# Performance work log

Measured on AMD Instinct MI355X. Metric: run time of the kernel, lower is better.

The kernel has to match this reference:

```python
import jax, jax.numpy as jnp
import numpy as np

N_NODES = 50000
N_EDGES = 800000
IN_DIM = 128
HID = 64
HEADS = 4
NEG_SLOPE = 0.2  # PyG GATConv default
EPS = 1e-16


def _glorot(key, shape):
    fan_in, fan_out = shape[0], shape[-1]
    lim = jnp.sqrt(6.0 / (fan_in + fan_out))
    return jax.random.uniform(key, shape, jnp.float32, -lim, lim)


def setup_inputs() -> dict:
    key = jax.random.key(0)
    ks = jax.random.split(key, 10)
    x = jax.random.normal(ks[0], (N_NODES, IN_DIM), jnp.float32)
    edge_index = jax.random.randint(ks[1], (2, N_EDGES), 0, N_NODES, jnp.int64)
    # Layer 1: in=128 -> 64 per head, 4 heads (concat -> 256)
    W1 = _glorot(ks[2], (IN_DIM, HEADS * HID))
    a_src1 = _glorot(ks[3], (HEADS, HID))
    a_dst1 = _glorot(ks[4], (HEADS, HID))
    b1 = jnp.zeros((HEADS * HID,), jnp.float32)
    # Layer 2: in=256 -> 1, 1 head
    W2 = _glorot(ks[5], (HEADS * HID, 1))
    a_src2 = _glorot(ks[6], (1, 1))
    a_dst2 = _glorot(ks[7], (1, 1))
    b2 = jnp.zeros((1,), jnp.float32)
    return {"x": x, "edge_index": edge_index, "W1": W1, "a_src1": a_src1,
            "a_dst1": a_dst1, "b1": b1, "W2": W2, "a_src2": a_src2,
            "a_dst2": a_dst2, "b2": b2}


def gat_conv(x, src, dst, W, a_src, a_dst, bias, heads, out_dim, num_nodes, concat):
    # Linear projection per head: [N, heads, out_dim]
    h = (x @ W).reshape(num_nodes, heads, out_dim)
    # Node-level attention logits: [N, heads]
    alpha_s = jnp.einsum('nhd,hd->nh', h, a_src)
    alpha_d = jnp.einsum('nhd,hd->nh', h, a_dst)
    # Per-edge score with LeakyReLU
    e = jax.nn.leaky_relu(alpha_s[src] + alpha_d[dst], NEG_SLOPE)  # [E, heads]
    # Segment softmax over incoming edges of each destination node
    e_max = jax.lax.stop_gradient(jax.ops.segment_max(e, dst, num_segments=num_nodes))
    e_exp = jnp.exp(e - e_max[dst])
    denom = jax.ops.segment_sum(e_exp, dst, num_segments=num_nodes)
    alpha = e_exp / (denom[dst] + EPS)  # [E, heads]
    # Weighted scatter-aggregate of source features
    msg = h[src] * alpha[:, :, None]  # [E, heads, out_dim]
    out = jax.ops.segment_sum(msg, dst, num_segments=num_nodes)
    if concat:
        out = out.reshape(num_nodes, heads * out_dim)
    else:
        out = out.mean(axis=1)
    return out + bias


def reference(x, edge_index, W1, a_src1, a_dst1, b1, W2, a_src2, a_dst2, b2):
    n = x.shape[0]
    loops = jnp.arange(n, dtype=edge_index.dtype)
    src = jnp.concatenate([edge_index[0], loops])  # PyG add_self_loops=True
    dst = jnp.concatenate([edge_index[1], loops])
    h = gat_conv(x, src, dst, W1, a_src1, a_dst1, b1, HEADS, HID, n, concat=True)
    h = jax.nn.relu(h)
    out = gat_conv(h, src, dst, W2, a_src2, a_dst2, b2, 1, 1, n, concat=True)
    return jax.nn.sigmoid(out)
```

## Files before the change

### kernel.cpp

```cpp
#include <hip/hip_runtime.h>
#include <hip/hip_bf16.h>

#define N_NODES 50000
#define N_EDGES 800000
#define ET      (N_EDGES + N_NODES)
#define IN_DIM  128
#define HID     64
#define HEADS   4
#define C1      (HEADS * HID)
#define NEG_SLOPE 0.2f

#define NBH     256
#define NBUCKET 196
#define SCAN_N  (NBUCKET * NBH)

typedef unsigned short ushort_t;
typedef __attribute__((ext_vector_type(8))) short bf16x8;
typedef __attribute__((ext_vector_type(4))) float f32x4;

__device__ __forceinline__ float asf(unsigned int u) {
    union { unsigned int i; float f; } c; c.i = u; return c.f;
}
__device__ __forceinline__ float bf2f(ushort_t u) {
    return asf(((unsigned int)u) << 16);
}
__device__ __forceinline__ ushort_t f2bf(float f) {
    union { float f; unsigned int i; } c; c.f = f;
    unsigned int r = c.i + 0x7fffu + ((c.i >> 16) & 1u);
    return (ushort_t)(r >> 16);
}
__device__ __forceinline__ float lrelu(float x) { return x > 0.f ? x : NEG_SLOPE * x; }

__device__ __forceinline__ float wave_sum(float v) {
    #pragma unroll
    for (int off = 32; off > 0; off >>= 1) v += __shfl_xor(v, off, 64);
    return v;
}
__device__ __forceinline__ int wave_sum_i(int v) {
    #pragma unroll
    for (int off = 32; off > 0; off >>= 1) v += __shfl_xor(v, off, 64);
    return v;
}

__device__ __forceinline__ int load_idx(const int* ei, int elem, int is64) {
    return is64 ? ei[2 * elem] : ei[elem];
}

__device__ __forceinline__ int detect64(const int* __restrict__ ei) {
    int lane = threadIdx.x & 63;
    unsigned long long nz = __ballot(lane < 32 && ei[2 * lane + 1] != 0);
    return nz == 0ull;
}

__global__ __launch_bounds__(256) void k_hist(const int* __restrict__ ei,
                                              int* __restrict__ HT,
                                              const float* __restrict__ W1,
                                              ushort_t* __restrict__ w1s) {
    __shared__ int lcnt[NBUCKET];
    int f = detect64(ei);
    if (threadIdx.x < NBUCKET) lcnt[threadIdx.x] = 0;
    if (threadIdx.x < 128) {
        int o = blockIdx.x * 128 + threadIdx.x;
        int j = o & 7, l = (o >> 3) & 63, c = (o >> 9) & 3, t = o >> 11;
        int k = c * 32 + ((l >> 4) << 3) + j;
        int n = (t << 4) + (l & 15);
        w1s[o] = f2bf(W1[k * C1 + n]);
    }
    __syncthreads();
    for (int e = blockIdx.x * 256 + threadIdx.x; e < ET; e += NBH * 256) {
        int d = (e < N_EDGES) ? load_idx(ei, N_EDGES + e, f) : e - N_EDGES;
        atomicAdd(&lcnt[d >> 8], 1);
    }
    __syncthreads();
    if (threadIdx.x < NBUCKET)
        HT[threadIdx.x * NBH + blockIdx.x] = lcnt[threadIdx.x];
}

__global__ __launch_bounds__(256) void k_blksum(const int* __restrict__ v,
                                                int* __restrict__ bsum) {
    int i = blockIdx.x * 256 + threadIdx.x;
    int s = wave_sum_i(v[i]);
    __shared__ int ws[4];
    int lane = threadIdx.x & 63, wid = threadIdx.x >> 6;
    if (lane == 0) ws[wid] = s;
    __syncthreads();
    if (threadIdx.x == 0) bsum[blockIdx.x] = ws[0] + ws[1] + ws[2] + ws[3];
}

__global__ __launch_bounds__(256) void k_bscan(const int* __restrict__ bsum,
                                               int* __restrict__ boff) {
    int tid = threadIdx.x, lane = tid & 63, wid = tid >> 6;
    int v = (tid < NBUCKET) ? bsum[tid] : 0;
    int x = v;
    #pragma unroll
    for (int off = 1; off < 64; off <<= 1) {
        int t = __shfl_up(x, off, 64);
        if (lane >= off) x += t;
    }
    __shared__ int ws[4];
    if (lane == 63) ws[wid] = x;
    __syncthreads();
    int add = 0;
    for (int w = 0; w < 4; ++w) if (w < wid) add += ws[w];
    x += add;
    if (tid < NBUCKET) boff[tid] = x - v;
}

__global__ __launch_bounds__(256) void k_apply(const int* __restrict__ v,
                                               const int* __restrict__ boff,
                                               int* __restrict__ out) {
    int i = blockIdx.x * 256 + threadIdx.x;
    int lane = threadIdx.x & 63, wid = threadIdx.x >> 6;
    int val = v[i];
    int x = val;
    #pragma unroll
    for (int off = 1; off < 64; off <<= 1) {
        int t = __shfl_up(x, off, 64);
        if (lane >= off) x += t;
    }
    __shared__ int ws[4];
    if (lane == 63) ws[wid] = x;
    __syncthreads();
    int add = boff[blockIdx.x];
    for (int w = 0; w < 4; ++w) if (w < wid) add += ws[w];
    out[i] = add + x - val;
}

__global__ __launch_bounds__(256) void k_bucket_scatter(const int* __restrict__ ei,
                                                        const int* __restrict__ HToff,
                                                        uint2* __restrict__ bucketed) {
    __shared__ int lbase[NBUCKET];
    int f = detect64(ei);
    if (threadIdx.x < NBUCKET)
        lbase[threadIdx.x] = HToff[threadIdx.x * NBH + blockIdx.x];
    __syncthreads();
    for (int e = blockIdx.x * 256 + threadIdx.x; e < ET; e += NBH * 256) {
        int s, d;
        if (e < N_EDGES) { s = load_idx(ei, e, f); d = load_idx(ei, N_EDGES + e, f); }
        else             { s = d = e - N_EDGES; }
        int pos = atomicAdd(&lbase[d >> 8], 1);
        bucketed[pos] = make_uint2((unsigned)s, (unsigned)d);
    }
}

__global__ __launch_bounds__(256) void k_fine(const uint2* __restrict__ bucketed,
                                              const int* __restrict__ HToff,
                                              int* __restrict__ row_start,
                                              int* __restrict__ edge_src) {
    __shared__ int fcnt[256];
    __shared__ int fcur[256];
    __shared__ int ws[4];
    int b = blockIdx.x, tid = threadIdx.x;
    int lane = tid & 63, wid = tid >> 6;
    int estart = HToff[b * NBH];
    int eend   = (b + 1 < NBUCKET) ? HToff[(b + 1) * NBH] : ET;
    fcnt[tid] = 0;
    __syncthreads();
    for (int i = estart + tid; i < eend; i += 256)
        atomicAdd(&fcnt[bucketed[i].y & 255], 1);
    __syncthreads();
    int v = fcnt[tid];
    int x = v;
    #pragma unroll
    for (int off = 1; off < 64; off <<= 1) {
        int t = __shfl_up(x, off, 64);
        if (lane >= off) x += t;
    }
    if (lane == 63) ws[wid] = x;
    __syncthreads();
    int add = 0;
    for (int w = 0; w < 4; ++w) if (w < wid) add += ws[w];
    int excl = add + x - v;
    int node = b * 256 + tid;
    if (node <= N_NODES) row_start[node] = estart + excl;
    fcur[tid] = estart + excl;
    __syncthreads();
    for (int i = estart + tid; i < eend; i += 256) {
        uint2 u = bucketed[i];
        int pos = atomicAdd(&fcur[u.y & 255], 1);
        edge_src[pos] = (int)u.x;
    }
}

__global__ __launch_bounds__(256) void k_gemm1(const float* __restrict__ x,
                                               const ushort_t* __restrict__ w1s,
                                               const float* __restrict__ a_src1,
                                               const float* __restrict__ a_dst1,
                                               ushort_t* __restrict__ h1,
                                               float* __restrict__ as1,
                                               float* __restrict__ ad1) {
    int lane = threadIdx.x & 63;
    int wave = (blockIdx.x * 256 + threadIdx.x) >> 6;
    int row0 = wave * 16;
    if (row0 >= N_NODES) return;
    int quad = lane >> 4, mrow = lane & 15;

    f32x4 acc[16];
    #pragma unroll
    for (int t = 0; t < 16; ++t) acc[t] = (f32x4){0.f, 0.f, 0.f, 0.f};

    const float* xrow = x + (size_t)(row0 + mrow) * IN_DIM + quad * 8;
    #pragma unroll
    for (int c = 0; c < 4; ++c) {
        float4 xa = *(const float4*)(xrow + c * 32);
        float4 xb = *(const float4*)(xrow + c * 32 + 4);
        bf16x8 a;
        a[0] = (short)f2bf(xa.x); a[1] = (short)f2bf(xa.y);
        a[2] = (short)f2bf(xa.z); a[3] = (short)f2bf(xa.w);
        a[4] = (short)f2bf(xb.x); a[5] = (short)f2bf(xb.y);
        a[6] = (short)f2bf(xb.z); a[7] = (short)f2bf(xb.w);
        #pragma unroll
        for (int t = 0; t < 16; ++t) {
            bf16x8 b = *(const bf16x8*)(w1s + (((t * 4 + c) * 64 + lane) << 3));
            acc[t] = __builtin_amdgcn_mfma_f32_16x16x32_bf16(a, b, acc[t], 0, 0, 0);
        }
    }

    #pragma unroll
    for (int t = 0; t < 16; ++t) {
        int col = t * 16 + mrow;
        #pragma unroll
        for (int r = 0; r < 4; ++r) {
            h1[(size_t)(row0 + quad * 4 + r) * C1 + col] = f2bf(acc[t][r]);
        }
    }

    float asv[16], adv[16];
    #pragma unroll
    for (int t = 0; t < 16; ++t) {
        asv[t] = a_src1[t * 16 + mrow];
        adv[t] = a_dst1[t * 16 + mrow];
    }
    #pragma unroll
    for (int r = 0; r < 4; ++r) {
        float ps[4] = {0.f, 0.f, 0.f, 0.f};
        float pd[4] = {0.f, 0.f, 0.f, 0.f};
        #pragma unroll
        for (int t = 0; t < 16; ++t) {
            ps[t >> 2] += acc[t][r] * asv[t];
            pd[t >> 2] += acc[t][r] * adv[t];
        }
        #pragma unroll
        for (int h = 0; h < 4; ++h) {
            #pragma unroll
            for (int off = 1; off < 16; off <<= 1) {
                ps[h] += __shfl_xor(ps[h], off, 64);
                pd[h] += __shfl_xor(pd[h], off, 64);
            }
        }
        if (mrow == 0) {
            int rr = row0 + quad * 4 + r;
            #pragma unroll
            for (int h = 0; h < 4; ++h) {
                as1[rr * 4 + h] = ps[h];
                ad1[rr * 4 + h] = pd[h];
            }
        }
    }
}

__global__ __launch_bounds__(256) void k_agg1(const ushort_t* __restrict__ h1,
                                              const float* __restrict__ as1,
                                              const float* __restrict__ ad1,
                                              const int* __restrict__ row_start,
                                              const int* __restrict__ edge_src,
                                              const float* __restrict__ b1,
                                              const float* __restrict__ W2,
                                              const float* __restrict__ a_src2,
                                              const float* __restrict__ a_dst2,
                                              float2* __restrict__ pk,
                                              float* __restrict__ ad2) {
    __shared__ float wbuf[4][64][4];
    int lane = threadIdx.x & 63;
    int wid  = threadIdx.x >> 6;
    int node = blockIdx.x * 4 + wid;
    int rs = row_start[node], re = row_start[node + 1];
    float4 ad = *(const float4*)&ad1[node * 4];
    const int lane32 = lane & 31;
    const int half   = lane >> 5;
    const int head8  = lane32 >> 3;

    float acc[8] = {0.f, 0.f, 0.f, 0.f, 0.f, 0.f, 0.f, 0.f};
    float4 den = make_float4(0.f, 0.f, 0.f, 0.f);

    for (int base = rs; base < re; base += 64) {
        int i = base + lane;
        int s_l = 0;
        float4 w = make_float4(0.f, 0.f, 0.f, 0.f);
        if (i < re) {
            s_l = edge_src[i];
            float4 av = *(const float4*)&as1[s_l * 4];
            w.x = __expf(lrelu(av.x + ad.x));
            w.y = __expf(lrelu(av.y + ad.y));
            w.z = __expf(lrelu(av.z + ad.z));
            w.w = __expf(lrelu(av.w + ad.w));
        }
        den.x += w.x; den.y += w.y; den.z += w.z; den.w += w.w;
        *(float4*)&wbuf[wid][lane][0] = w;
        int m = re - base; if (m > 64) m = 64;
        int j = 0;
        for (; j + 8 <= m; j += 8) {
            int sp[4]; uint4 pp[4]; float gg[4];
            #pragma unroll
            for (int q = 0; q < 4; ++q) {
                int s0 = __builtin_amdgcn_readlane(s_l, j + 2 * q);
                int s1 = __builtin_amdgcn_readlane(s_l, j + 2 * q + 1);
                sp[q] = half ? s1 : s0;
            }
            #pragma unroll
            for (int q = 0; q < 4; ++q) {
                pp[q] = *(const uint4*)(h1 + (size_t)sp[q] * C1 + lane32 * 8);
                gg[q] = wbuf[wid][j + 2 * q + half][head8];
            }
            #pragma unroll
            for (int q = 0; q < 4; ++q) {
                acc[0] += gg[q] * asf(pp[q].x << 16);
                acc[1] += gg[q] * asf(pp[q].x & 0xffff0000u);
                acc[2] += gg[q] * asf(pp[q].y << 16);
                acc[3] += gg[q] * asf(pp[q].y & 0xffff0000u);
                acc[4] += gg[q] * asf(pp[q].z << 16);
                acc[5] += gg[q] * asf(pp[q].z & 0xffff0000u);
                acc[6] += gg[q] * asf(pp[q].w << 16);
                acc[7] += gg[q] * asf(pp[q].w & 0xffff0000u);
            }
        }
        for (; j < m; j += 2) {
            int s0 = __builtin_amdgcn_readlane(s_l, j);
            int s1 = __builtin_amdgcn_readlane(s_l, j + 1);
            int sp = half ? s1 : s0;
            uint4 p0 = *(const uint4*)(h1 + (size_t)sp * C1 + lane32 * 8);
            float g0 = wbuf[wid][j + half][head8];
            acc[0] += g0 * asf(p0.x << 16);
            acc[1] += g0 * asf(p0.x & 0xffff0000u);
            acc[2] += g0 * asf(p0.y << 16);
            acc[3] += g0 * asf(p0.y & 0xffff0000u);
            acc[4] += g0 * asf(p0.z << 16);
            acc[5] += g0 * asf(p0.z & 0xffff0000u);
            acc[6] += g0 * asf(p0.w << 16);
            acc[7] += g0 * asf(p0.w & 0xffff0000u);
        }
    }

    #pragma unroll
    for (int i2 = 0; i2 < 8; ++i2) acc[i2] += __shfl_xor(acc[i2], 32, 64);

    float d0 = wave_sum(den.x), d1 = wave_sum(den.y);
    float d2 = wave_sum(den.z), d3 = wave_sum(den.w);
    float dh = head8 == 0 ? d0 : head8 == 1 ? d1 : head8 == 2 ? d2 : d3;
    float inv = 1.f / (dh + 1e-16f);
    float4 bva = *(const float4*)&b1[lane32 * 8];
    float4 bvb = *(const float4*)&b1[lane32 * 8 + 4];
    float o[8];
    o[0] = fmaxf(acc[0] * inv + bva.x, 0.f);
    o[1] = fmaxf(acc[1] * inv + bva.y, 0.f);
    o[2] = fmaxf(acc[2] * inv + bva.z, 0.f);
    o[3] = fmaxf(acc[3] * inv + bva.w, 0.f);
    o[4] = fmaxf(acc[4] * inv + bvb.x, 0.f);
    o[5] = fmaxf(acc[5] * inv + bvb.y, 0.f);
    o[6] = fmaxf(acc[6] * inv + bvb.z, 0.f);
    o[7] = fmaxf(acc[7] * inv + bvb.w, 0.f);
    float4 wva = *(const float4*)&W2[lane32 * 8];
    float4 wvb = *(const float4*)&W2[lane32 * 8 + 4];
    float sum = o[0] * wva.x + o[1] * wva.y + o[2] * wva.z + o[3] * wva.w
              + o[4] * wvb.x + o[5] * wvb.y + o[6] * wvb.z + o[7] * wvb.w;
    sum = wave_sum(sum) * 0.5f;
    if (lane == 0) {
        float2 p; p.x = sum * a_src2[0]; p.y = sum;
        pk[node]  = p;
        ad2[node] = sum * a_dst2[0];
    }
}

__global__ __launch_bounds__(256) void k_agg2(const float2* __restrict__ pk,
                                              const float* __restrict__ ad2,
                                              const int* __restrict__ row_start,
                                              const int* __restrict__ edge_src,
                                              const float* __restrict__ b2,
                                              float* __restrict__ outp) {
    int lane = threadIdx.x & 63;
    int node = blockIdx.x * 4 + (threadIdx.x >> 6);
    int rs = row_start[node], re = row_start[node + 1];
    float adv = ad2[node];
    float se = 0.f, wsm = 0.f;
    for (int i = rs + lane; i < re; i += 64) {
        int s = edge_src[i];
        float2 p = pk[s];
        float w = __expf(lrelu(p.x + adv));
        se += w; wsm += w * p.y;
    }
    se = wave_sum(se); wsm = wave_sum(wsm);
    if (lane == 0) {
        float v = wsm / (se + 1e-16f) + b2[0];
        outp[node] = 1.f / (1.f + __expf(-v));
    }
}

extern "C" void kernel_launch(void* const* d_in, const int* in_sizes, int n_in,
                              void* d_out, int out_size, void* d_ws, size_t ws_size,
                              hipStream_t stream) {
    (void)in_sizes; (void)n_in; (void)out_size; (void)ws_size;
    const float* x      = (const float*)d_in[0];
    const int*   ei     = (const int*)  d_in[1];
    const float* W1     = (const float*)d_in[2];
    const float* a_src1 = (const float*)d_in[3];
    const float* a_dst1 = (const float*)d_in[4];
    const float* b1     = (const float*)d_in[5];
    const float* W2     = (const float*)d_in[6];
    const float* a_src2 = (const float*)d_in[7];
    const float* a_dst2 = (const float*)d_in[8];
    const float* b2     = (const float*)d_in[9];
    float* out = (float*)d_out;

    char* w = (char*)d_ws;
    size_t off = 0;
    auto alloc = [&](size_t bytes) {
        void* p = w + off; off += (bytes + 255) & ~(size_t)255; return p;
    };
    ushort_t* h1       = (ushort_t*)alloc((size_t)N_NODES * C1 * 2);
    ushort_t* w1s      = (ushort_t*)alloc((size_t)IN_DIM * C1 * 2);
    float*    as1      = (float*)   alloc((size_t)N_NODES * 4 * 4);
    float*    ad1      = (float*)   alloc((size_t)N_NODES * 4 * 4);
    float2*   pk       = (float2*)  alloc((size_t)N_NODES * 8);
    float*    ad2      = (float*)   alloc((size_t)N_NODES * 4);
    int*      row_start= (int*)     alloc((size_t)(N_NODES + 1) * 4);
    int*      edge_src = (int*)     alloc((size_t)ET * 4);
    uint2*    bucketed = (uint2*)   alloc((size_t)ET * 8);
    int*      HT       = (int*)     alloc((size_t)SCAN_N * 4);
    int*      HToff    = (int*)     alloc((size_t)SCAN_N * 4);
    int*      bsum     = (int*)     alloc((size_t)NBUCKET * 4);
    int*      boff     = (int*)     alloc((size_t)NBUCKET * 4);

    k_hist<<<NBH, 256, 0, stream>>>(ei, HT, W1, w1s);
    k_blksum<<<NBUCKET, 256, 0, stream>>>(HT, bsum);
    k_bscan<<<1, 256, 0, stream>>>(bsum, boff);
    k_apply<<<NBUCKET, 256, 0, stream>>>(HT, boff, HToff);
    k_bucket_scatter<<<NBH, 256, 0, stream>>>(ei, HToff, bucketed);
    k_fine<<<NBUCKET, 256, 0, stream>>>(bucketed, HToff, row_start, edge_src);

    int nwave = (N_NODES + 15) / 16;
    k_gemm1<<<(nwave + 3) / 4, 256, 0, stream>>>(x, w1s, a_src1, a_dst1, h1, as1, ad1);
    k_agg1<<<N_NODES / 4, 256, 0, stream>>>(h1, as1, ad1, row_start, edge_src,
                                            b1, W2, a_src2, a_dst2, pk, ad2);
    k_agg2<<<N_NODES / 4, 256, 0, stream>>>(pk, ad2, row_start, edge_src, b2, out);
}
```

Baseline: 213.6 us.

## Split layer-1 aggregation across two blocks per node by head pairs

Each destination node is now handled by two waves in separate blocks, each covering two of the four heads (128 columns) with 4-byte gathers per lane instead of 16-byte gathers over half-wave edge pairs. Partial layer-2 projections are written per half and combined in the layer-2 aggregation kernel, which now applies a_src2/a_dst2 itself. The aim is more parallelism and less per-wave latency on high-degree nodes, at the cost of doubling edge_src/as1 reads and using narrower memory transactions.

```diff
diff --git a/kernel.cpp b/kernel.cpp
--- a/kernel.cpp
+++ b/kernel.cpp
@@ -266,127 +266,89 @@
                                               const int* __restrict__ edge_src,
                                               const float* __restrict__ b1,
                                               const float* __restrict__ W2,
-                                              const float* __restrict__ a_src2,
-                                              const float* __restrict__ a_dst2,
-                                              float2* __restrict__ pk,
-                                              float* __restrict__ ad2) {
-    __shared__ float wbuf[4][64][4];
+                                              float* __restrict__ pp) {
+    __shared__ float wbuf[4][64][2];
     int lane = threadIdx.x & 63;
     int wid  = threadIdx.x >> 6;
-    int node = blockIdx.x * 4 + wid;
+    int half = blockIdx.x & 1;
+    int node = (blockIdx.x >> 1) * 4 + wid;
     int rs = row_start[node], re = row_start[node + 1];
-    float4 ad = *(const float4*)&ad1[node * 4];
-    const int lane32 = lane & 31;
-    const int half   = lane >> 5;
-    const int head8  = lane32 >> 3;
-
-    float acc[8] = {0.f, 0.f, 0.f, 0.f, 0.f, 0.f, 0.f, 0.f};
-    float4 den = make_float4(0.f, 0.f, 0.f, 0.f);
+    float2 ad = *(const float2*)&ad1[node * 4 + 2 * half];
+    const int hsel = lane >> 5;
+    const int col0 = half * 128 + lane * 2;
+
+    float acc0 = 0.f, acc1 = 0.f;
+    float den0 = 0.f, den1 = 0.f;
 
     for (int base = rs; base < re; base += 64) {
         int i = base + lane;
         int s_l = 0;
-        float4 w = make_float4(0.f, 0.f, 0.f, 0.f);
+        float2 w = make_float2(0.f, 0.f);
         if (i < re) {
             s_l = edge_src[i];
-            float4 av = *(const float4*)&as1[s_l * 4];
+            float2 av = *(const float2*)&as1[s_l * 4 + 2 * half];
             w.x = __expf(lrelu(av.x + ad.x));
             w.y = __expf(lrelu(av.y + ad.y));
-            w.z = __expf(lrelu(av.z + ad.z));
-            w.w = __expf(lrelu(av.w + ad.w));
-        }
-        den.x += w.x; den.y += w.y; den.z += w.z; den.w += w.w;
-        *(float4*)&wbuf[wid][lane][0] = w;
+        }
+        den0 += w.x; den1 += w.y;
+        *(float2*)&wbuf[wid][lane][0] = w;
         int m = re - base; if (m > 64) m = 64;
         int j = 0;
         for (; j + 8 <= m; j += 8) {
-            int sp[4]; uint4 pp[4]; float gg[4];
+            int ss[8]; unsigned pq[8]; float gg[8];
             #pragma unroll
-            for (int q = 0; q < 4; ++q) {
-                int s0 = __builtin_amdgcn_readlane(s_l, j + 2 * q);
-                int s1 = __builtin_amdgcn_readlane(s_l, j + 2 * q + 1);
-                sp[q] = half ? s1 : s0;
+            for (int q = 0; q < 8; ++q) ss[q] = __builtin_amdgcn_readlane(s_l, j + q);
+            #pragma unroll
+            for (int q = 0; q < 8; ++q) {
+                pq[q] = *(const unsigned*)(h1 + (size_t)ss[q] * C1 + col0);
+                gg[q] = wbuf[wid][j + q][hsel];
             }
             #pragma unroll
-            for (int q = 0; q < 4; ++q) {
-                pp[q] = *(const uint4*)(h1 + (size_t)sp[q] * C1 + lane32 * 8);
-                gg[q] = wbuf[wid][j + 2 * q + half][head8];
+            for (int q = 0; q < 8; ++q) {
+                acc0 += gg[q] * asf(pq[q] << 16);
+                acc1 += gg[q] * asf(pq[q] & 0xffff0000u);
             }
-            #pragma unroll
-            for (int q = 0; q < 4; ++q) {
-                acc[0] += gg[q] * asf(pp[q].x << 16);
-                acc[1] += gg[q] * asf(pp[q].x & 0xffff0000u);
-                acc[2] += gg[q] * asf(pp[q].y << 16);
-                acc[3] += gg[q] * asf(pp[q].y & 0xffff0000u);
-                acc[4] += gg[q] * asf(pp[q].z << 16);
-                acc[5] += gg[q] * asf(pp[q].z & 0xffff0000u);
-                acc[6] += gg[q] * asf(pp[q].w << 16);
-                acc[7] += gg[q] * asf(pp[q].w & 0xffff0000u);
-            }
-        }
-        for (; j < m; j += 2) {
+        }
+        for (; j < m; ++j) {
             int s0 = __builtin_amdgcn_readlane(s_l, j);
-            int s1 = __builtin_amdgcn_readlane(s_l, j + 1);
-            int sp = half ? s1 : s0;
-            uint4 p0 = *(const uint4*)(h1 + (size_t)sp * C1 + lane32 * 8);
-            float g0 = wbuf[wid][j + half][head8];
-            acc[0] += g0 * asf(p0.x << 16);
-            acc[1] += g0 * asf(p0.x & 0xffff0000u);
-            acc[2] += g0 * asf(p0.y << 16);
-            acc[3] += g0 * asf(p0.y & 0xffff0000u);
-            acc[4] += g0 * asf(p0.z << 16);
-            acc[5] += g0 * asf(p0.z & 0xffff0000u);
-            acc[6] += g0 * asf(p0.w << 16);
-            acc[7] += g0 * asf(p0.w & 0xffff0000u);
-        }
-    }
-
-    #pragma unroll
-    for (int i2 = 0; i2 < 8; ++i2) acc[i2] += __shfl_xor(acc[i2], 32, 64);
-
-    float d0 = wave_sum(den.x), d1 = wave_sum(den.y);
-    float d2 = wave_sum(den.z), d3 = wave_sum(den.w);
-    float dh = head8 == 0 ? d0 : head8 == 1 ? d1 : head8 == 2 ? d2 : d3;
+            unsigned p0 = *(const unsigned*)(h1 + (size_t)s0 * C1 + col0);
+            float g0 = wbuf[wid][j][hsel];
+            acc0 += g0 * asf(p0 << 16);
+            acc1 += g0 * asf(p0 & 0xffff0000u);
+        }
+    }
+
+    float d0 = wave_sum(den0), d1 = wave_sum(den1);
+    float dh = hsel == 0 ? d0 : d1;
     float inv = 1.f / (dh + 1e-16f);
-    float4 bva = *(const float4*)&b1[lane32 * 8];
-    float4 bvb = *(const float4*)&b1[lane32 * 8 + 4];
-    float o[8];
-    o[0] = fmaxf(acc[0] * inv + bva.x, 0.f);
-    o[1] = fmaxf(acc[1] * inv + bva.y, 0.f);
-    o[2] = fmaxf(acc[2] * inv + bva.z, 0.f);
-    o[3] = fmaxf(acc[3] * inv + bva.w, 0.f);
-    o[4] = fmaxf(acc[4] * inv + bvb.x, 0.f);
-    o[5] = fmaxf(acc[5] * inv + bvb.y, 0.f);
-    o[6] = fmaxf(acc[6] * inv + bvb.z, 0.f);
-    o[7] = fmaxf(acc[7] * inv + bvb.w, 0.f);
-    float4 wva = *(const float4*)&W2[lane32 * 8];
-    float4 wvb = *(const float4*)&W2[lane32 * 8 + 4];
-    float sum = o[0] * wva.x + o[1] * wva.y + o[2] * wva.z + o[3] * wva.w
-              + o[4] * wvb.x + o[5] * wvb.y + o[6] * wvb.z + o[7] * wvb.w;
-    sum = wave_sum(sum) * 0.5f;
-    if (lane == 0) {
-        float2 p; p.x = sum * a_src2[0]; p.y = sum;
-        pk[node]  = p;
-        ad2[node] = sum * a_dst2[0];
-    }
-}
-
-__global__ __launch_bounds__(256) void k_agg2(const float2* __restrict__ pk,
-                                              const float* __restrict__ ad2,
+    float2 bv = *(const float2*)&b1[col0];
+    float o0 = fmaxf(acc0 * inv + bv.x, 0.f);
+    float o1 = fmaxf(acc1 * inv + bv.y, 0.f);
+    float2 wv = *(const float2*)&W2[col0];
+    float part = wave_sum(o0 * wv.x + o1 * wv.y);
+    if (lane == 0) pp[node * 2 + half] = part;
+}
+
+__global__ __launch_bounds__(256) void k_agg2(const float* __restrict__ pp,
                                               const int* __restrict__ row_start,
                                               const int* __restrict__ edge_src,
+                                              const float* __restrict__ a_src2,
+                                              const float* __restrict__ a_dst2,
                                               const float* __restrict__ b2,
                                               float* __restrict__ outp) {
     int lane = threadIdx.x & 63;
     int node = blockIdx.x * 4 + (threadIdx.x >> 6);
     int rs = row_start[node], re = row_start[node + 1];
-    float adv = ad2[node];
+    float as2v = a_src2[0];
+    float2 pd = *(const float2*)&pp[node * 2];
+    float adv = (pd.x + pd.y) * a_dst2[0];
     float se = 0.f, wsm = 0.f;
     for (int i = rs + lane; i < re; i += 64) {
         int s = edge_src[i];
-        float2 p = pk[s];
-        float w = __expf(lrelu(p.x + adv));
-        se += w; wsm += w * p.y;
+        float2 p = *(const float2*)&pp[s * 2];
+        float h2s = p.x + p.y;
+        float w = __expf(lrelu(h2s * as2v + adv));
+        se += w; wsm += w * h2s;
     }
     se = wave_sum(se); wsm = wave_sum(wsm);
     if (lane == 0) {
@@ -420,8 +382,7 @@
     ushort_t* w1s      = (ushort_t*)alloc((size_t)IN_DIM * C1 * 2);
     float*    as1      = (float*)   alloc((size_t)N_NODES * 4 * 4);
     float*    ad1      = (float*)   alloc((size_t)N_NODES * 4 * 4);
-    float2*   pk       = (float2*)  alloc((size_t)N_NODES * 8);
-    float*    ad2      = (float*)   alloc((size_t)N_NODES * 4);
+    float*    pp       = (float*)   alloc((size_t)N_NODES * 2 * 4);
     int*      row_start= (int*)     alloc((size_t)(N_NODES + 1) * 4);
     int*      edge_src = (int*)     alloc((size_t)ET * 4);
     uint2*    bucketed = (uint2*)   alloc((size_t)ET * 8);
@@ -439,7 +400,8 @@
 
     int nwave = (N_NODES + 15) / 16;
     k_gemm1<<<(nwave + 3) / 4, 256, 0, stream>>>(x, w1s, a_src1, a_dst1, h1, as1, ad1);
-    k_agg1<<<N_NODES / 4, 256, 0, stream>>>(h1, as1, ad1, row_start, edge_src,
-                                            b1, W2, a_src2, a_dst2, pk, ad2);
-    k_agg2<<<N_NODES / 4, 256, 0, stream>>>(pk, ad2, row_start, edge_src, b2, out);
-}
+    k_agg1<<<2 * (N_NODES / 4), 256, 0, stream>>>(h1, as1, ad1, row_start, edge_src,
+                                                  b1, W2, pp);
+    k_agg2<<<N_NODES / 4, 256, 0, stream>>>(pp, row_start, edge_src,
+                                            a_src2, a_dst2, b2, out);
+}
```

Result: slower. 220.7 us (+3.3%).
